# Kernel optimization log

Hardware: AMD Instinct MI355X
Metric: run time of the kernel (lower is better)

Reference implementation:

```python
import jax, jax.numpy as jnp
import numpy as np
from jax import lax

D = 256      # d_model
NH = 4       # nhead == len(multi_size)
DH = D // NH # per-head dim = 64
B, H, W = 8, 32, 32
EPS_LN = 1e-5
EPS_ATT = 1e-6


def conv2d(x, w, pad):
    # x: [B,C,H,W], w: [O,I,k,k], SAME padding via pad=k//2
    return lax.conv_general_dilated(
        x, w, window_strides=(1, 1), padding=[(pad, pad), (pad, pad)],
        dimension_numbers=("NCHW", "OIHW", "NCHW"))


def layer_norm(x, g, b):
    m = jnp.mean(x, axis=-1, keepdims=True)
    v = jnp.mean((x - m) ** 2, axis=-1, keepdims=True)
    return (x - m) * lax.rsqrt(v + EPS_LN) * g + b


def setup_inputs() -> dict:
    key = jax.random.key(0)
    ks = jax.random.split(key, 20)
    s = 0.02
    inp = {
        "x": jax.random.normal(ks[0], (B, D, H, W), jnp.float32),
        "source": jax.random.normal(ks[1], (B, D, H, W), jnp.float32),
        # q projection: conv3x3 d_model -> d_model (bias-free)
        "Wq": jax.random.normal(ks[2], (D, D, 3, 3), jnp.float32) * s,
        # MultiConv k projection: kernels 1,3,5,7, each d_model -> dim
        "Wk1": jax.random.normal(ks[3], (DH, D, 1, 1), jnp.float32) * s,
        "Wk3": jax.random.normal(ks[4], (DH, D, 3, 3), jnp.float32) * s,
        "Wk5": jax.random.normal(ks[5], (DH, D, 5, 5), jnp.float32) * s,
        "Wk7": jax.random.normal(ks[6], (DH, D, 7, 7), jnp.float32) * s,
        # MultiConv v projection
        "Wv1": jax.random.normal(ks[7], (DH, D, 1, 1), jnp.float32) * s,
        "Wv3": jax.random.normal(ks[8], (DH, D, 3, 3), jnp.float32) * s,
        "Wv5": jax.random.normal(ks[9], (DH, D, 5, 5), jnp.float32) * s,
        "Wv7": jax.random.normal(ks[10], (DH, D, 7, 7), jnp.float32) * s,
        # merge linear (bias=False), stored [in,out]
        "Wm": jax.random.normal(ks[11], (D, D), jnp.float32) * s,
        "ln1_g": jnp.ones((D,), jnp.float32),
        "ln1_b": jnp.zeros((D,), jnp.float32),
        "ln2_g": jnp.ones((D,), jnp.float32),
        "ln2_b": jnp.zeros((D,), jnp.float32),
        # FF mlp: Linear(2D->2D, no bias), ReLU, Linear(2D->D, no bias); [in,out]
        "W1": jax.random.normal(ks[12], (2 * D, 2 * D), jnp.float32) * s,
        "W2": jax.random.normal(ks[13], (2 * D, D), jnp.float32) * s,
    }
    return inp


def _forward(x, source, Wq, Wk1, Wk3, Wk5, Wk7, Wv1, Wv3, Wv5, Wv7,
             Wm, ln1_g, ln1_b, ln2_g, ln2_b, W1, W2):
    b, c, h, w = x.shape
    h1, w1 = source.shape[2], source.shape[3]
    L = h * w
    S = h1 * w1

    # projections (multi-scale convs -> heads along channel)
    q = conv2d(x, Wq, 1)                                        # [b,D,h,w]
    k = jnp.concatenate([conv2d(source, Wk1, 0), conv2d(source, Wk3, 1),
                         conv2d(source, Wk5, 2), conv2d(source, Wk7, 3)], axis=1)
    v = jnp.concatenate([conv2d(source, Wv1, 0), conv2d(source, Wv3, 1),
                         conv2d(source, Wv5, 2), conv2d(source, Wv7, 3)], axis=1)

    # b c h w -> b (h w) (nhead dim) -> b L nhead dim
    q = q.transpose(0, 2, 3, 1).reshape(b, L, NH, DH)
    k = k.transpose(0, 2, 3, 1).reshape(b, S, NH, DH)
    v = v.transpose(0, 2, 3, 1).reshape(b, S, NH, DH)

    # FullAttention_vis: softmax attention map [b, L, S, nhead]
    temp = DH ** -0.5
    qk = jnp.einsum("blhd,bshd->blsh", q, k)
    attn_vis = jax.nn.softmax(qk * temp, axis=2)

    # LinearAttention (elu+1 kernel feature map)
    Qf = jax.nn.elu(q) + 1.0
    Kf = jax.nn.elu(k) + 1.0
    v_len = jnp.float32(S)
    vals = v / v_len
    KV = jnp.einsum("bshd,bshv->bhdv", Kf, vals)                # [b,NH,DH,DH]
    Z = 1.0 / (jnp.einsum("blhd,bhd->blh", Qf, Kf.sum(axis=1)) + EPS_ATT)
    msg = jnp.einsum("blhd,bhdv,blh->blhv", Qf, KV, Z) * v_len  # [b,L,NH,DH]

    # merge + norm1
    msg = layer_norm(msg.reshape(b, L, D) @ Wm, ln1_g, ln1_b)

    # FF (mlp): cat -> Linear -> ReLU -> Linear -> norm2
    xf = x.transpose(0, 2, 3, 1).reshape(b, L, c)
    ff = jax.nn.relu(jnp.concatenate([xf, msg], axis=2) @ W1) @ W2
    msg = layer_norm(ff, ln2_g, ln2_b)                          # [b,L,D]
    msg = msg.reshape(b, h, w, c).transpose(0, 3, 1, 2)         # b c h w

    out = x + msg
    # b (h0 w0) (h1 w1) c -> b c h0 w0 h1 w1
    vis = attn_vis.reshape(b, h, w, h1, w1, NH).transpose(0, 5, 1, 2, 3, 4)
    return out, vis


def reference(x, source, Wq, Wk1, Wk3, Wk5, Wk7, Wv1, Wv3, Wv5, Wv7,
              Wm, ln1_g, ln1_b, ln2_g, ln2_b, W1, W2):
    return _forward(x, source, Wq, Wk1, Wk3, Wk5, Wk7, Wv1, Wv3, Wv5, Wv7,
                    Wm, ln1_g, ln1_b, ln2_g, ln2_b, W1, W2)
```

## Files before the change

kernel.cpp:

```cpp
#include <hip/hip_runtime.h>

#define DEV __device__ __forceinline__

typedef unsigned short u16;
typedef unsigned int u32;
typedef __bf16 bf16x8 __attribute__((ext_vector_type(8)));
typedef float f32x4 __attribute__((ext_vector_type(4)));

DEV float elu1(float x) { return x > 0.f ? x + 1.f : __expf(x); }

DEV u16 f2bf(float f) {
    union { float f; unsigned u; } v; v.f = f;
    unsigned r = v.u + 0x7fffu + ((v.u >> 16) & 1u);
    return (u16)(r >> 16);
}

DEV float bf2f(u16 h) {
    union { u32 u; float f; } v; v.u = ((u32)h) << 16; return v.f;
}

__global__ __launch_bounds__(256) void prep1_kernel(
    const float* __restrict__ Wq,
    const float* __restrict__ Wk1, const float* __restrict__ Wk3,
    const float* __restrict__ Wk5, const float* __restrict__ Wk7,
    const float* __restrict__ Wv1, const float* __restrict__ Wv3,
    const float* __restrict__ Wv5, const float* __restrict__ Wv7,
    u16* __restrict__ wpack,
    const float* __restrict__ x, const float* __restrict__ src,
    u16* __restrict__ xbh, u16* __restrict__ sbh)
{
    __shared__ float lds[32 * 129];
    const int t = threadIdx.x;
    if (blockIdx.x < 1632) {
        int gid = blockIdx.x * 256 + t;
        int frag = gid >> 6, l = gid & 63;
        const float* W; int K, ocbase = 0, rel;
        if (frag < 1152) {
            W = Wq; K = 3; int slot = frag / 288; rel = frag % 288; ocbase = slot * 64;
        } else {
            int f = frag - 1152; int side = f / 2688; f %= 2688;
            if (f < 32)        { W = side ? Wv1 : Wk1; K = 1; rel = f; }
            else if (f < 320)  { W = side ? Wv3 : Wk3; K = 3; rel = f - 32; }
            else if (f < 1120) { W = side ? Wv5 : Wk5; K = 5; rel = f - 320; }
            else               { W = side ? Wv7 : Wk7; K = 7; rel = f - 1120; }
        }
        int og = rel & 3, cc = (rel >> 2) & 7, tap = rel >> 5;
        int dy = tap / K, dx = tap % K;
        int oc = ocbase + og * 16 + (l & 15);
        int c0 = cc * 32 + (l >> 4) * 8;
        u16 pk[8];
#pragma unroll
        for (int j = 0; j < 8; ++j)
            pk[j] = f2bf(W[((size_t)(oc * 256 + c0 + j) * K + dy) * K + dx]);
        *(int4*)&wpack[(size_t)frag * 512 + l * 8] = *(const int4*)pk;
        return;
    }
    const int i = blockIdx.x - 1632;
    const int inp = i >> 9, rem = i & 511;
    const int b = rem >> 6, cc = (rem >> 3) & 7, pxb = rem & 7;
    const float* in = (inp ? src : x) + ((size_t)b * 256 + cc * 32) * 1024 + pxb * 128;
    u16* outp = (inp ? sbh : xbh) + (size_t)b * 262144 + (size_t)cc * 32768 + pxb * 128 * 32;
#pragma unroll
    for (int u = 0; u < 4; ++u) {
        int unit = t + u * 256;
        int r = unit >> 5, px4 = unit & 31;
        float4 v = *(const float4*)(in + (size_t)r * 1024 + px4 * 4);
        lds[r * 129 + px4 * 4 + 0] = v.x;
        lds[r * 129 + px4 * 4 + 1] = v.y;
        lds[r * 129 + px4 * 4 + 2] = v.z;
        lds[r * 129 + px4 * 4 + 3] = v.w;
    }
    __syncthreads();
#pragma unroll
    for (int u = 0; u < 2; ++u) {
        int unit = t + u * 256;
        int px = unit >> 2, cg = unit & 3;
        u16 pk[8];
#pragma unroll
        for (int j = 0; j < 8; ++j) pk[j] = f2bf(lds[(cg * 8 + j) * 129 + px]);
        *(int4*)&outp[px * 32 + cg * 8] = *(const int4*)pk;
    }
}

template<int K>
DEV void conv_mfma_body(const u16* __restrict__ srcb,
                        const u16* __restrict__ wsec,
                        u16* __restrict__ dst,
                        u16* Bt, int y0, int cch0, int ncc, int t)
{
    constexpr int P = K / 2;
    const int w = t >> 6, l = t & 63;
    const int chi = l >> 4, ln = l & 15;
    const int rowbase = chi * 22 + w * 2 + 3 - P;
    const int colbase = ln + 3 - P;
    f32x4 acc[4][4];
#pragma unroll
    for (int m = 0; m < 4; ++m)
#pragma unroll
        for (int n = 0; n < 4; ++n) acc[m][n] = (f32x4){0.f, 0.f, 0.f, 0.f};

    for (int cc = 0; cc < ncc; ++cc) {
        const int ccg = cch0 + cc;
        __syncthreads();
#pragma unroll
        for (int u = 0; u < 7; ++u) {
            int unit = t + (u << 9);
            if (unit < 2816) {
                int xv = unit & 31, r = unit >> 5;
                int yy = r % 22, ch = r / 22;
                int ygl = y0 - 3 + yy;
                int4 pk;
                if ((unsigned)ygl < 32u)
                    pk = *(const int4*)&srcb[(size_t)ccg * 32768 + (ygl * 32 + xv) * 32 + ch * 8];
                else
                    pk = (int4){0, 0, 0, 0};
                *(int4*)&Bt[((ch * 22 + yy) * 40 + xv + 3) * 8] = pk;
            } else if (unit < 3520) {
                int hu = unit - 2816;
                int hx = hu & 7; int xi = hx < 3 ? hx : hx + 32;
                int r = hu >> 3; int yy = r % 22, ch = r / 22;
                int4 z = {0, 0, 0, 0};
                *(int4*)&Bt[((ch * 22 + yy) * 40 + xi) * 8] = z;
            }
        }
        __syncthreads();
#pragma unroll
        for (int dy = 0; dy < K; ++dy) {
#pragma unroll
            for (int dx = 0; dx < K; ++dx) {
                const int tap = dy * K + dx;
                const u16* wp = wsec + ((size_t)(tap * 8 + ccg) * 4) * 512 + l * 8;
                bf16x8 a0 = *(const bf16x8*)(wp);
                bf16x8 a1 = *(const bf16x8*)(wp + 512);
                bf16x8 a2 = *(const bf16x8*)(wp + 1024);
                bf16x8 a3 = *(const bf16x8*)(wp + 1536);
                bf16x8 bf[4];
#pragma unroll
                for (int n = 0; n < 4; ++n) {
                    int row = rowbase + dy + (n >> 1);
                    int col = colbase + dx + (n & 1) * 16;
                    bf[n] = *(const bf16x8*)&Bt[(row * 40 + col) * 8];
                }
#pragma unroll
                for (int n = 0; n < 4; ++n) {
                    acc[0][n] = __builtin_amdgcn_mfma_f32_16x16x32_bf16(a0, bf[n], acc[0][n], 0, 0, 0);
                    acc[1][n] = __builtin_amdgcn_mfma_f32_16x16x32_bf16(a1, bf[n], acc[1][n], 0, 0, 0);
                    acc[2][n] = __builtin_amdgcn_mfma_f32_16x16x32_bf16(a2, bf[n], acc[2][n], 0, 0, 0);
                    acc[3][n] = __builtin_amdgcn_mfma_f32_16x16x32_bf16(a3, bf[n], acc[3][n], 0, 0, 0);
                }
            }
        }
    }
#pragma unroll
    for (int m = 0; m < 4; ++m)
#pragma unroll
        for (int n = 0; n < 4; ++n) {
            int y = y0 + w * 2 + (n >> 1);
            int px = y * 32 + (n & 1) * 16 + ln;
            int ocb = m * 16 + chi * 4;
            u16 pk[4];
#pragma unroll
            for (int r = 0; r < 4; ++r) pk[r] = f2bf(acc[m][n][r]);
            *(uint2*)&dst[(size_t)px * 64 + ocb] = *(const uint2*)pk;
        }
}

__global__ __launch_bounds__(512) void conv_mfma_kernel(
    const u16* __restrict__ xbh, const u16* __restrict__ sbh,
    const u16* __restrict__ wpack,
    u16* __restrict__ kbt, u16* __restrict__ vbt,
    u16* __restrict__ pq, u16* __restrict__ p3,
    u16* __restrict__ p5, u16* __restrict__ p7)
{
    __shared__ u16 Bt[4 * 22 * 40 * 8];
    const int bx = blockIdx.x, t = threadIdx.x;
    const int b = bx / 76, job = bx % 76;
    const int m = job & 1, j = job >> 1;
    if (j < 8) {
        int slot = j >> 1, cp = j & 1;
        conv_mfma_body<3>(xbh + (size_t)b * 262144,
                          wpack + (size_t)(slot * 288) * 512,
                          pq + ((size_t)((slot * 2 + cp) * 8 + b)) * 65536,
                          Bt, m * 16, cp * 4, 4, t);
        return;
    }
    const int s2 = j - 8;
    const int side = s2 / 15, jj = s2 % 15;
    const u16* sp = sbh + (size_t)b * 262144;
    u16* fin = side ? vbt : kbt;
    const size_t wkb = 1152 + (size_t)side * 2688;
    if (jj == 0) {
        conv_mfma_body<1>(sp, wpack + (wkb + 0) * 512,
                          fin + ((size_t)(b * 4 + 0)) * 65536, Bt, m * 16, 0, 8, t);
    } else if (jj < 3) {
        int cp = jj - 1;
        conv_mfma_body<3>(sp, wpack + (wkb + 32) * 512,
                          p3 + ((size_t)((side * 2 + cp) * 8 + b)) * 65536,
                          Bt, m * 16, cp * 4, 4, t);
    } else if (jj < 7) {
        int cp = jj - 3;
        conv_mfma_body<5>(sp, wpack + (wkb + 320) * 512,
                          p5 + ((size_t)((side * 4 + cp) * 8 + b)) * 65536,
                          Bt, m * 16, cp * 2, 2, t);
    } else {
        int cp = jj - 7;
        conv_mfma_body<7>(sp, wpack + (wkb + 1120) * 512,
                          p7 + ((size_t)((side * 8 + cp) * 8 + b)) * 65536,
                          Bt, m * 16, cp, 1, t);
    }
}

__global__ __launch_bounds__(256) void prep2_kernel(
    const u16* __restrict__ pq, const u16* __restrict__ p3,
    const u16* __restrict__ p5, const u16* __restrict__ p7,
    u16* __restrict__ qbt, u16* __restrict__ kbt, u16* __restrict__ vbt,
    const float* __restrict__ W1, const float* __restrict__ W2,
    const float* __restrict__ Wm,
    u16* __restrict__ w1p, u16* __restrict__ w2p, u16* __restrict__ wmp)
{
    const int t = threadIdx.x;
    if (blockIdx.x < 2560) {
        int gid = blockIdx.x * 256 + t;
        int u8 = gid & 8191;
        int img = gid >> 13;
        const u16* srcb; u16* outb; int parts;
        if (img < 32) {
            int sub = img >> 3, b_ = img & 7;
            parts = 2;
            srcb = pq + ((size_t)(sub * 2) * 8 + b_) * 65536;
            outb = qbt + ((size_t)(b_ * 4 + sub)) * 65536;
        } else if (img < 48) {
            int i2 = img - 32; int sub = i2 >> 3, b_ = i2 & 7;
            parts = 2;
            srcb = p3 + ((size_t)(sub * 2) * 8 + b_) * 65536;
            outb = (sub ? vbt : kbt) + ((size_t)(b_ * 4 + 1)) * 65536;
        } else if (img < 64) {
            int i2 = img - 48; int sub = i2 >> 3, b_ = i2 & 7;
            parts = 4;
            srcb = p5 + ((size_t)(sub * 4) * 8 + b_) * 65536;
            outb = (sub ? vbt : kbt) + ((size_t)(b_ * 4 + 2)) * 65536;
        } else {
            int i2 = img - 64; int sub = i2 >> 3, b_ = i2 & 7;
            parts = 8;
            srcb = p7 + ((size_t)(sub * 8) * 8 + b_) * 65536;
            outb = (sub ? vbt : kbt) + ((size_t)(b_ * 4 + 3)) * 65536;
        }
        float sacc[8];
#pragma unroll
        for (int e = 0; e < 8; ++e) sacc[e] = 0.f;
        for (int p = 0; p < parts; ++p) {
            int4 u = *(const int4*)&srcb[(size_t)p * 524288 + (size_t)u8 * 8];
            const u16* uu = (const u16*)&u;
#pragma unroll
            for (int e = 0; e < 8; ++e) sacc[e] += bf2f(uu[e]);
        }
        u16 pk[8];
#pragma unroll
        for (int e = 0; e < 8; ++e) pk[e] = f2bf(sacc[e]);
        *(int4*)&outb[(size_t)u8 * 8] = *(const int4*)pk;
        return;
    }
    int gid = (blockIdx.x - 2560) * 256 + t;
    int f = gid >> 6, l = gid & 63;
    if (f >= 896) return;
    u16 pk[8];
    if (f < 512) {
        int ks = f >> 5, nf = f & 31;
#pragma unroll
        for (int j = 0; j < 8; ++j)
            pk[j] = f2bf(W1[(size_t)(ks * 32 + (l >> 4) * 8 + j) * 512 + nf * 16 + (l & 15)]);
        *(int4*)&w1p[(size_t)f * 512 + l * 8] = *(const int4*)pk;
    } else if (f < 768) {
        int f2 = f - 512;
        int ks = f2 >> 4, nf = f2 & 15;
#pragma unroll
        for (int j = 0; j < 8; ++j)
            pk[j] = f2bf(W2[(size_t)(ks * 32 + (l >> 4) * 8 + j) * 256 + nf * 16 + (l & 15)]);
        *(int4*)&w2p[(size_t)f2 * 512 + l * 8] = *(const int4*)pk;
    } else {
        int f3 = f - 768;
        int ks = f3 >> 4, nf = f3 & 15;
#pragma unroll
        for (int j = 0; j < 8; ++j)
            pk[j] = f2bf(Wm[(size_t)(ks * 32 + (l >> 4) * 8 + j) * 256 + nf * 16 + (l & 15)]);
        *(int4*)&wmp[(size_t)f3 * 512 + l * 8] = *(const int4*)pk;
    }
}

__global__ __launch_bounds__(256) void prep3_kernel(
    const u16* __restrict__ kbt, const u16* __restrict__ vbt,
    float* __restrict__ KVp, float* __restrict__ Ksump)
{
    __shared__ float4 smem4[2112];
    float* Kt = (float*)smem4;
    float* Vt = (float*)(smem4 + 64 * 17);
    const int t = threadIdx.x;
    const int bx = blockIdx.x;
    const int b = bx >> 4, h = (bx >> 2) & 3, ch = bx & 3;
    const u16* kbase = kbt + ((size_t)(b * 4 + h) * 1024 + ch * 256) * 64;
    const u16* vbase = vbt + ((size_t)(b * 4 + h) * 1024 + ch * 256) * 64;
    const int d = t >> 2, v0 = (t & 3) * 16;
    float4 acc[4];
#pragma unroll
    for (int j = 0; j < 4; ++j) acc[j] = make_float4(0.f, 0.f, 0.f, 0.f);
    float ks = 0.f;
    for (int st = 0; st < 4; ++st) {
        __syncthreads();
        {
            int s = t >> 2, d0 = (t & 3) * 16;
            const u16* krow = kbase + (size_t)(st * 64 + s) * 64;
            const u16* vrow = vbase + (size_t)(st * 64 + s) * 64;
#pragma unroll
            for (int oo = 0; oo < 2; ++oo) {
                int4 k8 = *(const int4*)&krow[d0 + oo * 8];
                int4 v8 = *(const int4*)&vrow[d0 + oo * 8];
                const u16* ku = (const u16*)&k8;
                const u16* vu = (const u16*)&v8;
#pragma unroll
                for (int e = 0; e < 8; ++e) {
                    Kt[s * 68 + d0 + oo * 8 + e] = elu1(bf2f(ku[e]));
                    Vt[s * 64 + d0 + oo * 8 + e] = bf2f(vu[e]);
                }
            }
        }
        __syncthreads();
#pragma unroll 8
        for (int s = 0; s < 64; ++s) {
            float kf = Kt[s * 68 + d];
            const float4* vvp = (const float4*)(Vt + s * 64 + v0);
#pragma unroll
            for (int j = 0; j < 4; ++j) {
                float4 vv = vvp[j];
                acc[j].x += kf * vv.x; acc[j].y += kf * vv.y;
                acc[j].z += kf * vv.z; acc[j].w += kf * vv.w;
            }
        }
        if (t < 64) {
#pragma unroll 8
            for (int s = 0; s < 64; ++s) ks += Kt[s * 68 + t];
        }
    }
    float* op = KVp + ((size_t)((ch * 32 + b * 4 + h) * 64 + d)) * 64 + v0;
#pragma unroll
    for (int j = 0; j < 4; ++j) ((float4*)op)[j] = acc[j];
    if (t < 64) Ksump[(size_t)(ch * 32 + b * 4 + h) * 64 + t] = ks;
}

__global__ __launch_bounds__(512) void qk_sm_msg_kernel(
    const u16* __restrict__ qbt, const u16* __restrict__ kbt,
    float* __restrict__ vis,
    const float* __restrict__ KVp, const float* __restrict__ Ksump,
    float* __restrict__ msg)
{
    __shared__ float4 smem4[4178];
    const int t = threadIdx.x;
    if (blockIdx.x < 1024) {
        u16* kf = (u16*)smem4;
        u16* qf = (u16*)smem4 + 32 * 512;
        float* redM = (float*)((char*)smem4 + 36864);
        float* redS = redM + 256;
        const int bx = blockIdx.x;
        const int b = bx >> 7, h = (bx >> 5) & 3, l0 = (bx & 31) * 32;
        const u16* qtp = qbt + ((size_t)(b * 4 + h)) * 1024 * 64;
        const u16* ktp = kbt + ((size_t)(b * 4 + h)) * 1024 * 64;

        if (t < 256) {
            int r = t & 31, dblk = t >> 5;
            int4 pk = *(const int4*)&qtp[(size_t)(l0 + r) * 64 + dblk * 8];
            *(int4*)&qf[(((r >> 4) * 2 + (dblk >> 2)) * 64 + (dblk & 3) * 16 + (r & 15)) * 8] = pk;
        }
        __syncthreads();

        const int w = t >> 6, l = t & 63, ln = l & 15, lg = l >> 4;
        bf16x8 a[2][2];
#pragma unroll
        for (int fr = 0; fr < 2; ++fr)
#pragma unroll
            for (int ks = 0; ks < 2; ++ks)
                a[fr][ks] = *(const bf16x8*)&qf[((fr * 2 + ks) * 64 + l) * 8];

        f32x4 acc[2][4][2];
#pragma unroll
        for (int fr = 0; fr < 2; ++fr)
#pragma unroll
            for (int cc = 0; cc < 4; ++cc)
#pragma unroll
                for (int f = 0; f < 2; ++f) acc[fr][cc][f] = (f32x4){0.f, 0.f, 0.f, 0.f};

#pragma unroll
        for (int cc = 0; cc < 4; ++cc) {
            __syncthreads();
#pragma unroll
            for (int it = 0; it < 4; ++it) {
                int unit = it * 512 + t;
                int sl = unit & 255, dblk = unit >> 8;
                int4 pk = *(const int4*)&ktp[(size_t)(cc * 256 + sl) * 64 + dblk * 8];
                *(int4*)&kf[(((sl >> 4) * 2 + (dblk >> 2)) * 64 + (dblk & 3) * 16 + (sl & 15)) * 8] = pk;
            }
            __syncthreads();
#pragma unroll
            for (int f = 0; f < 2; ++f) {
                int fg = (w * 2 + f) * 2;
                bf16x8 b0 = *(const bf16x8*)&kf[((fg + 0) * 64 + l) * 8];
                bf16x8 b1 = *(const bf16x8*)&kf[((fg + 1) * 64 + l) * 8];
#pragma unroll
                for (int fr = 0; fr < 2; ++fr) {
                    acc[fr][cc][f] = __builtin_amdgcn_mfma_f32_16x16x32_bf16(a[fr][0], b0, acc[fr][cc][f], 0, 0, 0);
                    acc[fr][cc][f] = __builtin_amdgcn_mfma_f32_16x16x32_bf16(a[fr][1], b1, acc[fr][cc][f], 0, 0, 0);
                }
            }
        }

#pragma unroll
        for (int fr = 0; fr < 2; ++fr)
#pragma unroll
            for (int cc = 0; cc < 4; ++cc)
#pragma unroll
                for (int f = 0; f < 2; ++f)
#pragma unroll
                    for (int e = 0; e < 4; ++e) acc[fr][cc][f][e] *= 0.125f;

        float rmax[2][4];
#pragma unroll
        for (int fr = 0; fr < 2; ++fr)
#pragma unroll
            for (int reg = 0; reg < 4; ++reg) {
                float m = -1e30f;
#pragma unroll
                for (int cc = 0; cc < 4; ++cc)
#pragma unroll
                    for (int f = 0; f < 2; ++f) m = fmaxf(m, acc[fr][cc][f][reg]);
#pragma unroll
                for (int off = 1; off < 16; off <<= 1) m = fmaxf(m, __shfl_xor(m, off));
                if (ln == 0) redM[(fr * 16 + lg * 4 + reg) * 8 + w] = m;
                rmax[fr][reg] = m;
            }
        __syncthreads();
#pragma unroll
        for (int fr = 0; fr < 2; ++fr)
#pragma unroll
            for (int reg = 0; reg < 4; ++reg) {
                int r = fr * 16 + lg * 4 + reg;
                float m = redM[r * 8];
#pragma unroll
                for (int ww = 1; ww < 8; ++ww) m = fmaxf(m, redM[r * 8 + ww]);
                rmax[fr][reg] = m;
            }
#pragma unroll
        for (int fr = 0; fr < 2; ++fr)
#pragma unroll
            for (int reg = 0; reg < 4; ++reg) {
                float s = 0.f;
                float m = rmax[fr][reg];
#pragma unroll
                for (int cc = 0; cc < 4; ++cc)
#pragma unroll
                    for (int f = 0; f < 2; ++f) {
                        float e = __expf(acc[fr][cc][f][reg] - m);
                        acc[fr][cc][f][reg] = e;
                        s += e;
                    }
#pragma unroll
                for (int off = 1; off < 16; off <<= 1) s += __shfl_xor(s, off);
                if (ln == 0) redS[(fr * 16 + lg * 4 + reg) * 8 + w] = s;
            }
        __syncthreads();
        float invv[2][4];
#pragma unroll
        for (int fr = 0; fr < 2; ++fr)
#pragma unroll
            for (int reg = 0; reg < 4; ++reg) {
                int r = fr * 16 + lg * 4 + reg;
                float s = redS[r * 8] + redS[r * 8 + 1] + redS[r * 8 + 2] + redS[r * 8 + 3]
                        + redS[r * 8 + 4] + redS[r * 8 + 5] + redS[r * 8 + 6] + redS[r * 8 + 7];
                invv[fr][reg] = 1.f / s;
            }
        float* outT = (float*)smem4;
        float* visp = vis + (((size_t)(b * 4 + h)) << 20);
#pragma unroll
        for (int cc = 0; cc < 4; ++cc) {
            __syncthreads();
#pragma unroll
            for (int fr = 0; fr < 2; ++fr)
#pragma unroll
                for (int reg = 0; reg < 4; ++reg) {
                    int r = fr * 16 + lg * 4 + reg;
#pragma unroll
                    for (int f = 0; f < 2; ++f)
                        outT[r * 260 + w * 32 + f * 16 + ln] = acc[fr][cc][f][reg] * invv[fr][reg];
                }
            __syncthreads();
#pragma unroll
            for (int u = 0; u < 4; ++u) {
                int unit = u * 512 + t;
                int r = unit >> 6, c4 = unit & 63;
                f32x4 v = *(const f32x4*)&outT[r * 260 + c4 * 4];
                __builtin_nontemporal_store(v,
                    (f32x4*)&visp[(size_t)(l0 + r) * 1024 + cc * 256 + c4 * 4]);
            }
        }
        return;
    }
    float* kvl = (float*)smem4;
    float* ksl = (float*)smem4 + 4 * 4112;
    const int bx2 = blockIdx.x - 1024;
    const int b = bx2 >> 3, l0 = (bx2 & 7) * 128;
#pragma unroll
    for (int m = 0; m < 8; ++m) {
        int unit = t + (m << 9);
        int hh = unit >> 10, dd = (unit >> 4) & 63, v4 = unit & 15;
        float4 s = make_float4(0.f, 0.f, 0.f, 0.f);
#pragma unroll
        for (int ch = 0; ch < 4; ++ch) {
            float4 u = *(const float4*)&KVp[((size_t)(ch * 32 + b * 4)) * 4096 + (size_t)unit * 4];
            s.x += u.x; s.y += u.y; s.z += u.z; s.w += u.w;
        }
        *(float4*)&kvl[hh * 4112 + dd * 64 + v4 * 4] = s;
    }
    if (t < 256) {
        float s = 0.f;
#pragma unroll
        for (int ch = 0; ch < 4; ++ch)
            s += Ksump[(size_t)(ch * 32 + b * 4) * 64 + t];
        ksl[(t >> 6) * 65 + (t & 63)] = s;
    }
    __syncthreads();
    const int h = t & 3, l = l0 + (t >> 2);
    const u16* qrow = qbt + ((size_t)(b * 4 + h) * 1024 + l) * 64;
    float qf[64];
#pragma unroll
    for (int j8 = 0; j8 < 8; ++j8) {
        int4 pk = *(const int4*)&qrow[j8 * 8];
        const u16* pku = (const u16*)&pk;
#pragma unroll
        for (int e = 0; e < 8; ++e) qf[j8 * 8 + e] = elu1(bf2f(pku[e]));
    }
    float zd = 1e-6f;
#pragma unroll
    for (int dd = 0; dd < 64; ++dd) zd += qf[dd] * ksl[h * 65 + dd];
    const float Z = 1.f / zd;
    float* op = msg + ((size_t)(b * 1024 + l)) * 256 + h * 64;
    for (int c0 = 0; c0 < 64; c0 += 16) {
        float4 a[4];
#pragma unroll
        for (int j = 0; j < 4; ++j) a[j] = make_float4(0.f, 0.f, 0.f, 0.f);
#pragma unroll
        for (int dd = 0; dd < 64; ++dd) {
            float qv = qf[dd];
            const float4* kp = (const float4*)(kvl + h * 4112 + dd * 64 + c0);
#pragma unroll
            for (int j = 0; j < 4; ++j) {
                float4 kk = kp[j];
                a[j].x += qv * kk.x; a[j].y += qv * kk.y;
                a[j].z += qv * kk.z; a[j].w += qv * kk.w;
            }
        }
#pragma unroll
        for (int j = 0; j < 4; ++j) {
            a[j].x *= Z; a[j].y *= Z; a[j].z *= Z; a[j].w *= Z;
            ((float4*)(op + c0))[j] = a[j];
        }
    }
}

__global__ __launch_bounds__(256) void ff_fused_kernel(
    const float* __restrict__ x, const float* __restrict__ msg,
    const u16* __restrict__ wmp,
    const u16* __restrict__ w1p, const u16* __restrict__ w2p,
    const float* __restrict__ g1, const float* __restrict__ b1,
    const float* __restrict__ g2, const float* __restrict__ b2,
    float* __restrict__ out)
{
    __shared__ u16 tile[16 * 520];
    __shared__ u16 mtile[16 * 264];
    __shared__ float redS[16 * 4];
    __shared__ float redQ[16 * 4];
    float* tf = (float*)tile;
    const int t = threadIdx.x;
    const int base = blockIdx.x * 16;
    const int b = base >> 10, l0 = base & 1023;
    const int w = t >> 6, l = t & 63, ln = l & 15, lg = l >> 4;

    {
        int rr = t & 15, cg = t >> 4;
        for (int cci = 0; cci < 16; ++cci) {
            int c = cci * 16 + cg;
            tile[rr * 520 + c] = f2bf(x[((size_t)b * 256 + c) * 1024 + l0 + rr]);
        }
        int r = t >> 4, cb = (t & 15) * 16;
#pragma unroll
        for (int i = 0; i < 4; ++i) {
            float4 v = *(const float4*)&msg[((size_t)(base + r)) * 256 + cb + i * 4];
            u32 p0 = (u32)f2bf(v.x) | ((u32)f2bf(v.y) << 16);
            u32 p1 = (u32)f2bf(v.z) | ((u32)f2bf(v.w) << 16);
            *(u32*)&mtile[r * 264 + cb + i * 4] = p0;
            *(u32*)&mtile[r * 264 + cb + i * 4 + 2] = p1;
        }
    }
    __syncthreads();

    f32x4 accm[4];
#pragma unroll
    for (int fc = 0; fc < 4; ++fc) accm[fc] = (f32x4){0.f, 0.f, 0.f, 0.f};
    for (int ks = 0; ks < 8; ++ks) {
        bf16x8 a0 = *(const bf16x8*)&mtile[ln * 264 + ks * 32 + lg * 8];
#pragma unroll
        for (int fc = 0; fc < 4; ++fc) {
            bf16x8 bb = *(const bf16x8*)&wmp[((size_t)(ks * 16 + w * 4 + fc) * 64 + l) * 8];
            accm[fc] = __builtin_amdgcn_mfma_f32_16x16x32_bf16(a0, bb, accm[fc], 0, 0, 0);
        }
    }
#pragma unroll
    for (int reg = 0; reg < 4; ++reg) {
        float s = 0.f, qsum = 0.f;
#pragma unroll
        for (int fc = 0; fc < 4; ++fc) {
            float v = accm[fc][reg];
            s += v; qsum += v * v;
        }
#pragma unroll
        for (int off = 1; off < 16; off <<= 1) {
            s += __shfl_xor(s, off);
            qsum += __shfl_xor(qsum, off);
        }
        if (ln == 0) {
            int r = lg * 4 + reg;
            redS[r * 4 + w] = s;
            redQ[r * 4 + w] = qsum;
        }
    }
    __syncthreads();
#pragma unroll
    for (int fc = 0; fc < 4; ++fc) {
        int c = w * 64 + fc * 16 + ln;
        float gg = g1[c], bb = b1[c];
#pragma unroll
        for (int reg = 0; reg < 4; ++reg) {
            int r = lg * 4 + reg;
            float s = redS[r * 4] + redS[r * 4 + 1] + redS[r * 4 + 2] + redS[r * 4 + 3];
            float qs = redQ[r * 4] + redQ[r * 4 + 1] + redQ[r * 4 + 2] + redQ[r * 4 + 3];
            float mean = s * (1.f / 256.f);
            float rstd = rsqrtf(qs * (1.f / 256.f) - mean * mean + 1e-5f);
            tile[r * 520 + 256 + c] = f2bf((accm[fc][reg] - mean) * rstd * gg + bb);
        }
    }
    __syncthreads();

    f32x4 acc1[8];
#pragma unroll
    for (int fc = 0; fc < 8; ++fc) acc1[fc] = (f32x4){0.f, 0.f, 0.f, 0.f};
    for (int ks = 0; ks < 16; ++ks) {
        bf16x8 a0 = *(const bf16x8*)&tile[ln * 520 + ks * 32 + lg * 8];
#pragma unroll
        for (int fc = 0; fc < 8; ++fc) {
            bf16x8 bb = *(const bf16x8*)&w1p[((size_t)(ks * 32 + w * 8 + fc) * 64 + l) * 8];
            acc1[fc] = __builtin_amdgcn_mfma_f32_16x16x32_bf16(a0, bb, acc1[fc], 0, 0, 0);
        }
    }
    __syncthreads();
#pragma unroll
    for (int fc = 0; fc < 8; ++fc)
#pragma unroll
        for (int reg = 0; reg < 4; ++reg) {
            int r = lg * 4 + reg;
            int c = w * 128 + fc * 16 + ln;
            tile[r * 520 + c] = f2bf(fmaxf(acc1[fc][reg], 0.f));
        }
    __syncthreads();

    f32x4 acc2[4];
#pragma unroll
    for (int fc = 0; fc < 4; ++fc) acc2[fc] = (f32x4){0.f, 0.f, 0.f, 0.f};
    for (int ks = 0; ks < 16; ++ks) {
        bf16x8 a0 = *(const bf16x8*)&tile[ln * 520 + ks * 32 + lg * 8];
#pragma unroll
        for (int fc = 0; fc < 4; ++fc) {
            bf16x8 bb = *(const bf16x8*)&w2p[((size_t)(ks * 16 + w * 4 + fc) * 64 + l) * 8];
            acc2[fc] = __builtin_amdgcn_mfma_f32_16x16x32_bf16(a0, bb, acc2[fc], 0, 0, 0);
        }
    }
#pragma unroll
    for (int reg = 0; reg < 4; ++reg) {
        float s = 0.f, qsum = 0.f;
#pragma unroll
        for (int fc = 0; fc < 4; ++fc) {
            float v = acc2[fc][reg];
            s += v; qsum += v * v;
        }
#pragma unroll
        for (int off = 1; off < 16; off <<= 1) {
            s += __shfl_xor(s, off);
            qsum += __shfl_xor(qsum, off);
        }
        if (ln == 0) {
            int r = lg * 4 + reg;
            redS[r * 4 + w] = s;
            redQ[r * 4 + w] = qsum;
        }
    }
    __syncthreads();
    float mean[4], rstd[4];
#pragma unroll
    for (int reg = 0; reg < 4; ++reg) {
        int r = lg * 4 + reg;
        float s = redS[r * 4] + redS[r * 4 + 1] + redS[r * 4 + 2] + redS[r * 4 + 3];
        float qs = redQ[r * 4] + redQ[r * 4 + 1] + redQ[r * 4 + 2] + redQ[r * 4 + 3];
        float m = s * (1.f / 256.f);
        mean[reg] = m;
        rstd[reg] = rsqrtf(qs * (1.f / 256.f) - m * m + 1e-5f);
    }
    __syncthreads();
#pragma unroll
    for (int fc = 0; fc < 4; ++fc) {
        int c = w * 64 + fc * 16 + ln;
        float gg = g2[c], bb = b2[c];
#pragma unroll
        for (int reg = 0; reg < 4; ++reg) {
            int r = lg * 4 + reg;
            tf[r * 260 + c] = (acc2[fc][reg] - mean[reg]) * rstd[reg] * gg + bb;
        }
    }
    __syncthreads();
    {
        const float* xp = x + ((size_t)b * 256 + t) * 1024 + l0;
        float* op = out + ((size_t)b * 256 + t) * 1024 + l0;
#pragma unroll
        for (int i = 0; i < 4; ++i) {
            float4 xv = *(const float4*)(xp + i * 4);
            float4 o;
            o.x = xv.x + tf[(i * 4 + 0) * 260 + t];
            o.y = xv.y + tf[(i * 4 + 1) * 260 + t];
            o.z = xv.z + tf[(i * 4 + 2) * 260 + t];
            o.w = xv.w + tf[(i * 4 + 3) * 260 + t];
            *(float4*)(op + i * 4) = o;
        }
    }
}

extern "C" void kernel_launch(void* const* d_in, const int* in_sizes, int n_in,
                              void* d_out, int out_size, void* d_ws, size_t ws_size,
                              hipStream_t stream)
{
    const float* x    = (const float*)d_in[0];
    const float* src  = (const float*)d_in[1];
    const float* Wq   = (const float*)d_in[2];
    const float* Wk1  = (const float*)d_in[3];
    const float* Wk3  = (const float*)d_in[4];
    const float* Wk5  = (const float*)d_in[5];
    const float* Wk7  = (const float*)d_in[6];
    const float* Wv1  = (const float*)d_in[7];
    const float* Wv3  = (const float*)d_in[8];
    const float* Wv5  = (const float*)d_in[9];
    const float* Wv7  = (const float*)d_in[10];
    const float* Wm   = (const float*)d_in[11];
    const float* g1   = (const float*)d_in[12];
    const float* b1   = (const float*)d_in[13];
    const float* g2   = (const float*)d_in[14];
    const float* b2   = (const float*)d_in[15];
    const float* W1   = (const float*)d_in[16];
    const float* W2   = (const float*)d_in[17];

    float* out = (float*)d_out;
    float* vis = out + 2097152;

    u16* pq = (u16*)vis;
    u16* p3 = pq + 4194304;
    u16* p5 = p3 + 2097152;
    u16* p7 = p5 + 4194304;

    float* ws    = (float*)d_ws;
    u16*   qbt   = (u16*)ws;
    u16*   kbt   = (u16*)(ws + 1048576);
    u16*   vbt   = (u16*)(ws + 2097152);
    u16*   wpack = (u16*)(ws + 6291456);
    u16*   w1p   = (u16*)(ws + 6291456);
    u16*   w2p   = (u16*)(ws + 6422528);
    u16*   wmp   = (u16*)(ws + 6488064);
    u16*   xbh   = (u16*)(ws + 7962624);
    u16*   sbh   = (u16*)(ws + 9011200);
    float* msg   = ws + 10059776;
    float* KVp   = ws + 12156928;
    float* Ksump = ws + 12681216;

    prep1_kernel    <<<2656, 256, 0, stream>>>(Wq, Wk1, Wk3, Wk5, Wk7,
                                               Wv1, Wv3, Wv5, Wv7, wpack,
                                               x, src, xbh, sbh);
    conv_mfma_kernel<<<608,  512, 0, stream>>>(xbh, sbh, wpack, kbt, vbt,
                                               pq, p3, p5, p7);
    prep2_kernel    <<<2784, 256, 0, stream>>>(pq, p3, p5, p7, qbt, kbt, vbt,
                                               W1, W2, Wm, w1p, w2p, wmp);
    prep3_kernel    <<<128,  256, 0, stream>>>(kbt, vbt, KVp, Ksump);
    qk_sm_msg_kernel<<<1088, 512, 0, stream>>>(qbt, kbt, vis, KVp, Ksump, msg);
    ff_fused_kernel <<<512,  256, 0, stream>>>(x, msg, wmp, w1p, w2p,
                                               g1, b1, g2, b2, out);
}
```

Baseline: 255.2 us.

## Shrink shared memory in qk/msg kernel by processing heads in two passes

The message branch of the fused kernel now stages KV for two heads at a time over two passes, instead of all four heads at once. This roughly halves the kernel's static shared memory, which should allow more resident blocks per CU for both the softmax branch and the message branch. The softmax normalization now computes row inverses once into shared memory instead of in every thread's registers, which cuts register pressure at the cost of an extra barrier. The message branch uses fewer, larger blocks (32 instead of 64) that each loop twice with additional syncs.

```diff
diff --git a/kernel.cpp b/kernel.cpp
--- a/kernel.cpp
+++ b/kernel.cpp
@@ -352,7 +352,7 @@
     const float* __restrict__ KVp, const float* __restrict__ Ksump,
     float* __restrict__ msg)
 {
-    __shared__ float4 smem4[4178];
+    __shared__ float4 smem4[2432];
     const int t = threadIdx.x;
     if (blockIdx.x < 1024) {
         u16* kf = (u16*)smem4;
@@ -465,16 +465,13 @@
                 if (ln == 0) redS[(fr * 16 + lg * 4 + reg) * 8 + w] = s;
             }
         __syncthreads();
-        float invv[2][4];
-#pragma unroll
-        for (int fr = 0; fr < 2; ++fr)
-#pragma unroll
-            for (int reg = 0; reg < 4; ++reg) {
-                int r = fr * 16 + lg * 4 + reg;
-                float s = redS[r * 8] + redS[r * 8 + 1] + redS[r * 8 + 2] + redS[r * 8 + 3]
-                        + redS[r * 8 + 4] + redS[r * 8 + 5] + redS[r * 8 + 6] + redS[r * 8 + 7];
-                invv[fr][reg] = 1.f / s;
-            }
+        if (t < 32) {
+            float s = 0.f;
+#pragma unroll
+            for (int ww = 0; ww < 8; ++ww) s += redS[t * 8 + ww];
+            redM[t] = 1.f / s;
+        }
+        __syncthreads();
         float* outT = (float*)smem4;
         float* visp = vis + (((size_t)(b * 4 + h)) << 20);
 #pragma unroll
@@ -485,9 +482,10 @@
 #pragma unroll
                 for (int reg = 0; reg < 4; ++reg) {
                     int r = fr * 16 + lg * 4 + reg;
+                    float inv = redM[r];
 #pragma unroll
                     for (int f = 0; f < 2; ++f)
-                        outT[r * 260 + w * 32 + f * 16 + ln] = acc[fr][cc][f][reg] * invv[fr][reg];
+                        outT[r * 260 + w * 32 + f * 16 + ln] = acc[fr][cc][f][reg] * inv;
                 }
             __syncthreads();
 #pragma unroll
@@ -502,63 +500,69 @@
         return;
     }
     float* kvl = (float*)smem4;
-    float* ksl = (float*)smem4 + 4 * 4112;
+    float* ksl = (float*)smem4 + 2 * 4112;
     const int bx2 = blockIdx.x - 1024;
-    const int b = bx2 >> 3, l0 = (bx2 & 7) * 128;
-#pragma unroll
-    for (int m = 0; m < 8; ++m) {
-        int unit = t + (m << 9);
-        int hh = unit >> 10, dd = (unit >> 4) & 63, v4 = unit & 15;
-        float4 s = make_float4(0.f, 0.f, 0.f, 0.f);
-#pragma unroll
-        for (int ch = 0; ch < 4; ++ch) {
-            float4 u = *(const float4*)&KVp[((size_t)(ch * 32 + b * 4)) * 4096 + (size_t)unit * 4];
-            s.x += u.x; s.y += u.y; s.z += u.z; s.w += u.w;
-        }
-        *(float4*)&kvl[hh * 4112 + dd * 64 + v4 * 4] = s;
-    }
-    if (t < 256) {
-        float s = 0.f;
-#pragma unroll
-        for (int ch = 0; ch < 4; ++ch)
-            s += Ksump[(size_t)(ch * 32 + b * 4) * 64 + t];
-        ksl[(t >> 6) * 65 + (t & 63)] = s;
-    }
-    __syncthreads();
-    const int h = t & 3, l = l0 + (t >> 2);
-    const u16* qrow = qbt + ((size_t)(b * 4 + h) * 1024 + l) * 64;
-    float qf[64];
-#pragma unroll
-    for (int j8 = 0; j8 < 8; ++j8) {
-        int4 pk = *(const int4*)&qrow[j8 * 8];
-        const u16* pku = (const u16*)&pk;
-#pragma unroll
-        for (int e = 0; e < 8; ++e) qf[j8 * 8 + e] = elu1(bf2f(pku[e]));
-    }
-    float zd = 1e-6f;
-#pragma unroll
-    for (int dd = 0; dd < 64; ++dd) zd += qf[dd] * ksl[h * 65 + dd];
-    const float Z = 1.f / zd;
-    float* op = msg + ((size_t)(b * 1024 + l)) * 256 + h * 64;
-    for (int c0 = 0; c0 < 64; c0 += 16) {
-        float4 a[4];
-#pragma unroll
-        for (int j = 0; j < 4; ++j) a[j] = make_float4(0.f, 0.f, 0.f, 0.f);
-#pragma unroll
-        for (int dd = 0; dd < 64; ++dd) {
-            float qv = qf[dd];
-            const float4* kp = (const float4*)(kvl + h * 4112 + dd * 64 + c0);
+    const int b = bx2 >> 2, l0 = (bx2 & 3) * 256;
+    const int hoff = t & 1, lrow = l0 + (t >> 1);
+    for (int p = 0; p < 2; ++p) {
+        __syncthreads();
+#pragma unroll
+        for (int m = 0; m < 4; ++m) {
+            int unit = t + (m << 9);
+            int hh = unit >> 10, rem = unit & 1023;
+            int dd = rem >> 4, v4 = rem & 15;
+            float4 s = make_float4(0.f, 0.f, 0.f, 0.f);
+#pragma unroll
+            for (int ch = 0; ch < 4; ++ch) {
+                float4 u = *(const float4*)&KVp[((size_t)(ch * 32 + b * 4 + 2 * p + hh)) * 4096 + (size_t)rem * 4];
+                s.x += u.x; s.y += u.y; s.z += u.z; s.w += u.w;
+            }
+            *(float4*)&kvl[hh * 4112 + dd * 64 + v4 * 4] = s;
+        }
+        if (t < 128) {
+            int hh = t >> 6, dd = t & 63;
+            float s = 0.f;
+#pragma unroll
+            for (int ch = 0; ch < 4; ++ch)
+                s += Ksump[(size_t)(ch * 32 + b * 4 + 2 * p + hh) * 64 + dd];
+            ksl[hh * 65 + dd] = s;
+        }
+        __syncthreads();
+        const int h = 2 * p + hoff;
+        const u16* qrow = qbt + ((size_t)(b * 4 + h) * 1024 + lrow) * 64;
+        float qf[64];
+#pragma unroll
+        for (int j8 = 0; j8 < 8; ++j8) {
+            int4 pk = *(const int4*)&qrow[j8 * 8];
+            const u16* pku = (const u16*)&pk;
+#pragma unroll
+            for (int e = 0; e < 8; ++e) qf[j8 * 8 + e] = elu1(bf2f(pku[e]));
+        }
+        float zd = 1e-6f;
+#pragma unroll
+        for (int dd = 0; dd < 64; ++dd) zd += qf[dd] * ksl[hoff * 65 + dd];
+        const float Z = 1.f / zd;
+        float* op = msg + ((size_t)(b * 1024 + lrow)) * 256 + h * 64;
+        for (int c0 = 0; c0 < 64; c0 += 16) {
+            float4 a[4];
+#pragma unroll
+            for (int j = 0; j < 4; ++j) a[j] = make_float4(0.f, 0.f, 0.f, 0.f);
+#pragma unroll
+            for (int dd = 0; dd < 64; ++dd) {
+                float qv = qf[dd];
+                const float4* kp = (const float4*)(kvl + hoff * 4112 + dd * 64 + c0);
+#pragma unroll
+                for (int j = 0; j < 4; ++j) {
+                    float4 kk = kp[j];
+                    a[j].x += qv * kk.x; a[j].y += qv * kk.y;
+                    a[j].z += qv * kk.z; a[j].w += qv * kk.w;
+                }
+            }
 #pragma unroll
             for (int j = 0; j < 4; ++j) {
-                float4 kk = kp[j];
-                a[j].x += qv * kk.x; a[j].y += qv * kk.y;
-                a[j].z += qv * kk.z; a[j].w += qv * kk.w;
-            }
-        }
-#pragma unroll
-        for (int j = 0; j < 4; ++j) {
-            a[j].x *= Z; a[j].y *= Z; a[j].z *= Z; a[j].w *= Z;
-            ((float4*)(op + c0))[j] = a[j];
+                a[j].x *= Z; a[j].y *= Z; a[j].z *= Z; a[j].w *= Z;
+                ((float4*)(op + c0))[j] = a[j];
+            }
         }
     }
 }
@@ -790,7 +794,7 @@
     prep2_kernel    <<<2784, 256, 0, stream>>>(pq, p3, p5, p7, qbt, kbt, vbt,
                                                W1, W2, Wm, w1p, w2p, wmp);
     prep3_kernel    <<<128,  256, 0, stream>>>(kbt, vbt, KVp, Ksump);
-    qk_sm_msg_kernel<<<1088, 512, 0, stream>>>(qbt, kbt, vis, KVp, Ksump, msg);
+    qk_sm_msg_kernel<<<1056, 512, 0, stream>>>(qbt, kbt, vis, KVp, Ksump, msg);
     ff_fused_kernel <<<512,  256, 0, stream>>>(x, msg, wmp, w1p, w2p,
                                                g1, b1, g2, b2, out);
 }
```

Measured after the change: 275.7 us. +8.0%, slower.
